# Optimization experiments

Hardware: AMD Instinct MI355X
Metric: run time of the kernel (lower is better)

The kernel has to match this reference:

```python
import jax, jax.numpy as jnp
import numpy as np

B, D, UNITS, T, M = 16384, 256, 256, 32, 64


def hard_sigmoid(x):
    # keras hard_sigmoid: clip(0.2*x + 0.5, 0, 1)
    return jnp.clip(0.2 * x + 0.5, 0.0, 1.0)


def setup_inputs() -> dict:
    key = jax.random.key(0)
    ks = jax.random.split(key, 11)
    inputs = jax.random.normal(ks[0], (B, D), jnp.float32)
    h_tm1 = jax.random.normal(ks[1], (B, UNITS), jnp.float32)
    c_tm1 = jax.random.normal(ks[2], (B, UNITS), jnp.float32)
    h_tm2 = jax.random.normal(ks[3], (B, UNITS), jnp.float32)
    c_tm2 = jax.random.normal(ks[4], (B, UNITS), jnp.float32)
    neighbors = jax.random.randint(ks[5], (B, T, M), 0, 2, jnp.int32)      # binary adjacency rows
    mapping = jax.random.randint(ks[6], (B, M), 0, T, jnp.int32)           # processing time of each node
    reverse_mapping = jax.random.randint(ks[7], (B, T), 0, T, jnp.int32)   # time -> row index in neighbors
    W = jax.random.normal(ks[8], (D, 4 * UNITS), jnp.float32) * 0.05
    U = jax.random.normal(ks[9], (UNITS, 4 * UNITS), jnp.float32) * 0.05
    Un = jax.random.normal(ks[10], (UNITS, 4 * UNITS), jnp.float32) * 0.05
    # unit_forget_bias: zeros for i, ones for f, zeros for c and o
    bias = jnp.concatenate([jnp.zeros((UNITS,)), jnp.ones((UNITS,)), jnp.zeros((2 * UNITS,))]).astype(jnp.float32)
    return {"inputs": inputs, "h_tm1": h_tm1, "c_tm1": c_tm1, "h_tm2": h_tm2, "c_tm2": c_tm2,
            "neighbors": neighbors, "mapping": mapping, "reverse_mapping": reverse_mapping,
            "time": 16, "W": W, "U": U, "Un": Un, "bias": bias}


def reference(inputs, h_tm1, c_tm1, h_tm2, c_tm2, neighbors, mapping, reverse_mapping, time, W, U, Un, bias):
    # --- neighbor row gather: ng_rows[b] = neighbors[b, reverse_mapping[b, time]] ---
    prev_pos = reverse_mapping[:, time]                                      # [B]
    ng_rows = jnp.take_along_axis(neighbors, prev_pos[:, None, None], axis=1)[:, 0, :]  # [B, M]
    ng_f = ng_rows.astype(jnp.float32)
    is_past = (mapping < time).astype(jnp.float32)                           # [B, M]
    ng_num = jnp.sum(ng_f, axis=-1)                                          # [B]
    cnt_past = jnp.sum(ng_f * is_past, axis=-1)                              # [B]
    cnt_fut = ng_num - cnt_past                                              # [B]
    denom = jnp.where(ng_num > 0, ng_num, 1.0)
    has_ng = (ng_num > 0)[:, None]

    # original sums the FULL-batch state for each neighbor (K.sum over axes [0,1]),
    # so aggregation collapses to count_past*sum(h_tm1) + count_fut*sum(h_tm2), div_no_nan by ng_num.
    hs1 = jnp.sum(h_tm1, axis=0)                                             # [units]
    hs2 = jnp.sum(h_tm2, axis=0)
    ngs = jnp.where(has_ng,
                    (cnt_past[:, None] * hs1[None, :] + cnt_fut[:, None] * hs2[None, :]) / denom[:, None],
                    0.0)                                                     # [B, units]

    # --- gates (implementation=1, no dropout) ---
    z_x = inputs @ W + bias                                                  # [B, 4*units]
    x_i, x_f, x_c, x_o = jnp.split(z_x, 4, axis=-1)                          # x_f_avg == x_f in source
    U_i, U_f, U_c, U_o = jnp.split(U, 4, axis=-1)
    Un_i, Un_f, Un_c, Un_o = jnp.split(Un, 4, axis=-1)

    i = hard_sigmoid(x_i + h_tm1 @ U_i + ngs @ Un_i)
    f_avg = hard_sigmoid(x_f + h_tm1 @ Un_f)   # note: uses Un_f per source
    f = hard_sigmoid(x_f + h_tm1 @ U_f)
    c = jnp.tanh(x_c + h_tm1 @ U_c + ngs @ Un_c)
    o = hard_sigmoid(x_o + h_tm1 @ U_o + ngs @ Un_o)

    # --- neighbor memory aggregation: same batch-summed structure with f_avg*c ---
    m1 = jnp.sum(f_avg * c_tm1, axis=0)                                      # [units]
    m2 = jnp.sum(f_avg * c_tm2, axis=0)
    mem_agg = jnp.where(has_ng,
                        (cnt_past[:, None] * m1[None, :] + cnt_fut[:, None] * m2[None, :]) / denom[:, None],
                        0.0)                                                 # [B, units]

    memory = mem_agg + f * c_tm1 + i * c
    h = o * jnp.tanh(memory)
    return h, memory
```

## Files before the change

### kernel.cpp

```cpp
#include <hip/hip_runtime.h>
#include <cmath>

#define BB 16384
#define DD 256
#define UU 256
#define TT 32
#define MM 64

#define WS_ALPHA 0
#define WS_BETA  16384
#define WS_M1    32768
#define WS_M2    33024
#define WS_V1    33280
#define WS_V2    34304
#define WS_PART1 35328
#define WS_PART2 68096
#define WS_BF16_BYTE 403456

typedef short bf16x8 __attribute__((ext_vector_type(8)));
typedef float f32x16 __attribute__((ext_vector_type(16)));

__device__ __forceinline__ float hsig(float x) {
    return fminf(1.0f, fmaxf(0.0f, fmaf(0.2f, x, 0.5f)));
}
__device__ __forceinline__ short f2bf(float x) {
    unsigned u = __float_as_uint(x);
    unsigned r = (u + 0x7fffu + ((u >> 16) & 1u)) >> 16;
    return (short)r;
}
__device__ __forceinline__ float bf2f(short h) {
    return __uint_as_float(((unsigned)(unsigned short)h) << 16);
}

__global__ void k_prep(const float* __restrict__ inputs, const float* __restrict__ h1,
                       const float* __restrict__ h2,
                       const int* __restrict__ neighbors, const int* __restrict__ mapping,
                       const int* __restrict__ revmap, const int* __restrict__ timep,
                       const float* __restrict__ W, const float* __restrict__ U,
                       const float* __restrict__ Un,
                       short* __restrict__ Ahi, short* __restrict__ Alo,
                       short* __restrict__ Bg,
                       float* __restrict__ alpha, float* __restrict__ beta,
                       float* __restrict__ part1, float* __restrict__ part2) {
    int blk = blockIdx.x;
    int tid = threadIdx.x;
    if (blk < 4096) {
        int q = tid & 3;
        int m = (blk & 255) * 64 + (tid >> 2);
        int kc = blk >> 8;
        int s = q >> 1, h = q & 1;
        int k0 = kc * 32 + s * 16 + h * 4;
        const float* src = (k0 < 256) ? (inputs + m * 256 + k0) : (h1 + m * 256 + k0 - 256);
        float4 x0 = *(const float4*)(src);
        float4 x1 = *(const float4*)(src + 8);
        float xs[8] = {x0.x, x0.y, x0.z, x0.w, x1.x, x1.y, x1.z, x1.w};
        bf16x8 hv, lv;
        #pragma unroll
        for (int j = 0; j < 8; j++) {
            short hh = f2bf(xs[j]);
            hv[j] = hh;
            lv[j] = f2bf(xs[j] - bf2f(hh));
        }
        long doff = ((long)kc * 16384 + m) * 32 + q * 8;
        *(bf16x8*)(Ahi + doff) = hv;
        *(bf16x8*)(Alo + doff) = lv;
    } else if (blk < 4416) {
        int t = (blk - 4096) * 256 + tid;
        int lane = t & 63;
        int rest = t >> 6;
        int gs = rest % 10;
        int img = rest / 10;
        int g = gs >> 1, s = gs & 1;
        int nb = img >> 4, kc = img & 15;
        int u = nb * 32 + (lane & 31);
        int hl = lane >> 5;
        int c = (g < 4) ? g * 256 + u : 256 + u;
        bf16x8 hv, lv;
        #pragma unroll
        for (int j = 0; j < 8; j++) {
            int k = kc * 32 + s * 16 + hl * 4 + (j & 3) + 8 * (j >> 2);
            const float* sp;
            if (k < 256) sp = W + k * 1024 + c;
            else         sp = ((g < 4) ? U : Un) + (k - 256) * 1024 + c;
            float x = *sp;
            short hh = f2bf(x);
            hv[j] = hh;
            lv[j] = f2bf(x - bf2f(hh));
        }
        short* dst = Bg + (long)img * 10240 + gs * 512 + lane * 8;
        *(bf16x8*)dst = hv;
        *(bf16x8*)(dst + 5120) = lv;
    } else if (blk < 8512) {
        int lane = tid & 63;
        int wid  = tid >> 6;
        int b = (blk - 4416) * 4 + wid;
        int t = timep[0];
        int p = revmap[b * TT + t];
        int ng = neighbors[(b * TT + p) * MM + lane];
        int mp = mapping[b * MM + lane];
        int cnt = ng;
        int cp  = (mp < t) ? ng : 0;
        #pragma unroll
        for (int off = 32; off > 0; off >>= 1) {
            cnt += __shfl_xor(cnt, off);
            cp  += __shfl_xor(cp, off);
        }
        if (lane == 0) {
            float a = 0.f, be = 0.f;
            if (cnt > 0) {
                float inv = 1.0f / (float)cnt;
                a  = (float)cp * inv;
                be = (float)(cnt - cp) * inv;
            }
            alpha[b] = a;
            beta[b]  = be;
        }
    } else {
        int p = blk - 8512;
        int r0 = p * 128;
        float s1 = 0.f, s2 = 0.f;
        for (int r = 0; r < 128; r++) {
            s1 += h1[(r0 + r) * UU + tid];
            s2 += h2[(r0 + r) * UU + tid];
        }
        part1[p * 256 + tid] = s1;
        part2[p * 256 + tid] = s2;
    }
}

__global__ void k_mid(const float* __restrict__ Un,
                      const float* __restrict__ part1, const float* __restrict__ part2,
                      float* __restrict__ v1, float* __restrict__ v2,
                      float* __restrict__ m12) {
    __shared__ float sh1[256], sh2[256];
    int tid = threadIdx.x;
    if (blockIdx.x == 0 && tid < 512) m12[tid] = 0.f;
    float s1 = 0.f, s2 = 0.f;
    #pragma unroll 8
    for (int p = 0; p < 128; p++) {
        s1 += part1[p * 256 + tid];
        s2 += part2[p * 256 + tid];
    }
    sh1[tid] = s1;
    sh2[tid] = s2;
    __syncthreads();
    int j = blockIdx.x * 256 + tid;
    float a1 = 0.f, a2 = 0.f;
    for (int k = 0; k < 256; k++) {
        float w = Un[k * 1024 + j];
        a1 = fmaf(sh1[k], w, a1);
        a2 = fmaf(sh2[k], w, a2);
    }
    v1[j] = a1;
    v2[j] = a2;
}

#define STAGE_B(KC, BUF) { \
    const char* _s = (const char*)(Bt + (long)(KC) * 10240); \
    char* _d = (char*)(&Bs[BUF][0]); \
    _Pragma("unroll") \
    for (int _c = 0; _c < 5; _c++) { \
        int _u = wv * 5120 + _c * 1024; \
        __builtin_amdgcn_global_load_lds( \
            (const __attribute__((address_space(1))) void*)(_s + _u + lane * 16), \
            (__attribute__((address_space(3))) void*)(_d + _u), 16, 0, 0); \
    } }

__global__ __launch_bounds__(256) void k_gemm_mfma(
    const short* __restrict__ Ahi, const short* __restrict__ Alo,
    const short* __restrict__ Bg,
    const float* __restrict__ c1p, const float* __restrict__ c2p,
    const float* __restrict__ bias,
    const float* __restrict__ alpha, const float* __restrict__ beta,
    const float* __restrict__ v1, const float* __restrict__ v2,
    float* __restrict__ m1, float* __restrict__ m2,
    float* __restrict__ out_h, float* __restrict__ out_mem)
{
    __shared__ short Bs[2][10240];

    const int tid = threadIdx.x;
    const int lane = tid & 63;
    const int wv = tid >> 6;
    const int mb = blockIdx.x;
    const int nb = blockIdx.y;
    const int m0 = mb * 128;
    const short* Bt = Bg + (long)nb * 163840;

    const int col = lane & 31;
    const int hl = lane >> 5;
    const int m = m0 + wv * 32 + col;
    const long abase = (long)m * 32 + hl * 8;

    f32x16 acc[5];
    #pragma unroll
    for (int g = 0; g < 5; g++)
        #pragma unroll
        for (int r = 0; r < 16; r++) acc[g][r] = 0.f;

    STAGE_B(0, 0);
    bf16x8 ah0 = *(const bf16x8*)(Ahi + abase);
    bf16x8 ah1 = *(const bf16x8*)(Ahi + abase + 16);
    bf16x8 al0 = *(const bf16x8*)(Alo + abase);
    bf16x8 al1 = *(const bf16x8*)(Alo + abase + 16);

    for (int kc = 0; kc < 16; kc++) {
        __syncthreads();
        bf16x8 nh0, nh1, nl0, nl1;
        if (kc + 1 < 16) {
            STAGE_B(kc + 1, (kc + 1) & 1);
            long ab = abase + (long)(kc + 1) * 524288;
            nh0 = *(const bf16x8*)(Ahi + ab);
            nh1 = *(const bf16x8*)(Ahi + ab + 16);
            nl0 = *(const bf16x8*)(Alo + ab);
            nl1 = *(const bf16x8*)(Alo + ab + 16);
        }

        const char* bp = (const char*)Bs + (kc & 1) * 20480 + lane * 16;
        #pragma unroll
        for (int g = 0; g < 5; g++) {
            bf16x8 bh0 = *(const bf16x8*)(bp + (g * 2 + 0) * 1024);
            bf16x8 bh1 = *(const bf16x8*)(bp + (g * 2 + 1) * 1024);
            bf16x8 bl0 = *(const bf16x8*)(bp + 10240 + (g * 2 + 0) * 1024);
            bf16x8 bl1 = *(const bf16x8*)(bp + 10240 + (g * 2 + 1) * 1024);
            acc[g] = __builtin_amdgcn_mfma_f32_32x32x16_bf16(ah0, bh0, acc[g], 0, 0, 0);
            acc[g] = __builtin_amdgcn_mfma_f32_32x32x16_bf16(ah1, bh1, acc[g], 0, 0, 0);
            acc[g] = __builtin_amdgcn_mfma_f32_32x32x16_bf16(al0, bh0, acc[g], 0, 0, 0);
            acc[g] = __builtin_amdgcn_mfma_f32_32x32x16_bf16(al1, bh1, acc[g], 0, 0, 0);
            acc[g] = __builtin_amdgcn_mfma_f32_32x32x16_bf16(ah0, bl0, acc[g], 0, 0, 0);
            acc[g] = __builtin_amdgcn_mfma_f32_32x32x16_bf16(ah1, bl1, acc[g], 0, 0, 0);
        }
        if (kc + 1 < 16) { ah0 = nh0; ah1 = nh1; al0 = nl0; al1 = nl1; }
    }

    int u = nb * 32 + col;
    float bi = bias[u], bfv = bias[256 + u], bc = bias[512 + u], bo = bias[768 + u];
    float v1i = v1[u], v1c = v1[512 + u], v1o = v1[768 + u];
    float v2i = v2[u], v2c = v2[512 + u], v2o = v2[768 + u];

    float pm1 = 0.f, pm2 = 0.f;
    #pragma unroll
    for (int r = 0; r < 16; r++) {
        int row = (r & 3) + 8 * (r >> 2) + 4 * hl;
        int b = m0 + wv * 32 + row;
        float al = alpha[b], be = beta[b];
        float c1 = c1p[b * 256 + u];
        float c2 = c2p[b * 256 + u];
        float zi  = acc[0][r] + bi + al * v1i + be * v2i;
        float zf  = acc[1][r] + bfv;
        float zc  = acc[2][r] + bc + al * v1c + be * v2c;
        float zo  = acc[3][r] + bo + al * v1o + be * v2o;
        float zfa = acc[4][r] + bfv;
        float ig = hsig(zi), fg = hsig(zf), og = hsig(zo), fav = hsig(zfa);
        float cg = tanhf(zc);
        out_mem[b * 256 + u] = fg * c1 + ig * cg;
        out_h[b * 256 + u]  = og;
        pm1 += fav * c1;
        pm2 += fav * c2;
    }

    pm1 += __shfl_xor(pm1, 32);
    pm2 += __shfl_xor(pm2, 32);
    __syncthreads();
    float* red = (float*)&Bs[0][0];
    if (hl == 0) {
        red[(wv * 2 + 0) * 32 + col] = pm1;
        red[(wv * 2 + 1) * 32 + col] = pm2;
    }
    __syncthreads();
    if (tid < 64) {
        int d = tid >> 5, ui = tid & 31;
        float s = 0.f;
        #pragma unroll
        for (int w = 0; w < 4; w++) s += red[(w * 2 + d) * 32 + ui];
        atomicAdd(((d == 0) ? m1 : m2) + nb * 32 + ui, s);
    }
}

__global__ void k_final(const float* __restrict__ alpha, const float* __restrict__ beta,
                        const float* __restrict__ m1, const float* __restrict__ m2,
                        float* __restrict__ out_h, float* __restrict__ out_mem) {
    int idx = blockIdx.x * 256 + threadIdx.x;
    int b  = idx >> 6;
    int uv = idx & 63;
    float4 mp = ((const float4*)out_mem)[idx];
    float4 ov = ((const float4*)out_h)[idx];
    float al = alpha[b], be = beta[b];
    float4 m1v = ((const float4*)m1)[uv];
    float4 m2v = ((const float4*)m2)[uv];
    float4 mem, h;
    mem.x = fmaf(al, m1v.x, fmaf(be, m2v.x, mp.x)); h.x = ov.x * tanhf(mem.x);
    mem.y = fmaf(al, m1v.y, fmaf(be, m2v.y, mp.y)); h.y = ov.y * tanhf(mem.y);
    mem.z = fmaf(al, m1v.z, fmaf(be, m2v.z, mp.z)); h.z = ov.z * tanhf(mem.z);
    mem.w = fmaf(al, m1v.w, fmaf(be, m2v.w, mp.w)); h.w = ov.w * tanhf(mem.w);
    ((float4*)out_mem)[idx] = mem;
    ((float4*)out_h)[idx]   = h;
}

extern "C" void kernel_launch(void* const* d_in, const int* in_sizes, int n_in,
                              void* d_out, int out_size, void* d_ws, size_t ws_size,
                              hipStream_t stream) {
    const float* inputs   = (const float*)d_in[0];
    const float* h_tm1    = (const float*)d_in[1];
    const float* c_tm1    = (const float*)d_in[2];
    const float* h_tm2    = (const float*)d_in[3];
    const float* c_tm2    = (const float*)d_in[4];
    const int*   neighbors= (const int*)d_in[5];
    const int*   mapping  = (const int*)d_in[6];
    const int*   revmap   = (const int*)d_in[7];
    const int*   timep    = (const int*)d_in[8];
    const float* W        = (const float*)d_in[9];
    const float* Uw       = (const float*)d_in[10];
    const float* Un       = (const float*)d_in[11];
    const float* bias     = (const float*)d_in[12];

    float* ws    = (float*)d_ws;
    float* alpha = ws + WS_ALPHA;
    float* beta  = ws + WS_BETA;
    float* m1    = ws + WS_M1;
    float* m2    = ws + WS_M2;
    float* v1    = ws + WS_V1;
    float* v2    = ws + WS_V2;
    float* part1 = ws + WS_PART1;
    float* part2 = ws + WS_PART2;

    short* Ahi = (short*)((char*)d_ws + WS_BF16_BYTE);
    short* Alo = Ahi + 8388608;
    short* Bg  = Alo + 8388608;

    float* out_h   = (float*)d_out;
    float* out_mem = out_h + BB * UU;

    k_prep<<<8640, 256, 0, stream>>>(inputs, h_tm1, h_tm2, neighbors, mapping, revmap,
                                     timep, W, Uw, Un, Ahi, Alo, Bg, alpha, beta,
                                     part1, part2);
    k_mid<<<4, 256, 0, stream>>>(Un, part1, part2, v1, v2, m1);

    dim3 g3(128, 8);
    k_gemm_mfma<<<g3, 256, 0, stream>>>(Ahi, Alo, Bg, c_tm1, c_tm2, bias,
                                        alpha, beta, v1, v2, m1, m2, out_h, out_mem);

    k_final<<<BB * UU / 4 / 256, 256, 0, stream>>>(alpha, beta, m1, m2, out_h, out_mem);
}
```

Before: 361.7 us.

## Interleave MFMA accumulators and replace syncthreads with explicit vmcnt waits

Reorders the inner k-loop so consecutive MFMAs target the five independent accumulators rather than issuing six dependent MFMAs into the same accumulator, which hides MFMA result latency. LDS B-fragment reads are split into batches that are loaded ahead of the MFMAs consuming them. The full __syncthreads is replaced by explicit s_waitcnt vmcnt counts plus s_barrier, with sched_barriers pinning the order of loads. This lets prefetched A global loads stay in flight across the barrier. The hand-chosen vmcnt values depend on exactly how many memory ops STAGE_B issues, and a miscount could cause stale-data races.

```diff
diff --git a/kernel.cpp b/kernel.cpp
--- a/kernel.cpp
+++ b/kernel.cpp
@@ -198,37 +198,93 @@
         for (int r = 0; r < 16; r++) acc[g][r] = 0.f;
 
     STAGE_B(0, 0);
+    __builtin_amdgcn_sched_barrier(0);
     bf16x8 ah0 = *(const bf16x8*)(Ahi + abase);
     bf16x8 ah1 = *(const bf16x8*)(Ahi + abase + 16);
     bf16x8 al0 = *(const bf16x8*)(Alo + abase);
     bf16x8 al1 = *(const bf16x8*)(Alo + abase + 16);
+    __builtin_amdgcn_sched_barrier(0);
 
     for (int kc = 0; kc < 16; kc++) {
-        __syncthreads();
+        asm volatile("s_waitcnt vmcnt(4)" ::: "memory");
+        __builtin_amdgcn_s_barrier();
+
         bf16x8 nh0, nh1, nl0, nl1;
         if (kc + 1 < 16) {
             STAGE_B(kc + 1, (kc + 1) & 1);
+            __builtin_amdgcn_sched_barrier(0);
             long ab = abase + (long)(kc + 1) * 524288;
             nh0 = *(const bf16x8*)(Ahi + ab);
             nh1 = *(const bf16x8*)(Ahi + ab + 16);
             nl0 = *(const bf16x8*)(Alo + ab);
             nl1 = *(const bf16x8*)(Alo + ab + 16);
+            __builtin_amdgcn_sched_barrier(0);
+            asm volatile("s_waitcnt vmcnt(9)" ::: "memory");
+        } else {
+            asm volatile("s_waitcnt vmcnt(0)" ::: "memory");
         }
 
         const char* bp = (const char*)Bs + (kc & 1) * 20480 + lane * 16;
-        #pragma unroll
-        for (int g = 0; g < 5; g++) {
-            bf16x8 bh0 = *(const bf16x8*)(bp + (g * 2 + 0) * 1024);
-            bf16x8 bh1 = *(const bf16x8*)(bp + (g * 2 + 1) * 1024);
-            bf16x8 bl0 = *(const bf16x8*)(bp + 10240 + (g * 2 + 0) * 1024);
-            bf16x8 bl1 = *(const bf16x8*)(bp + 10240 + (g * 2 + 1) * 1024);
-            acc[g] = __builtin_amdgcn_mfma_f32_32x32x16_bf16(ah0, bh0, acc[g], 0, 0, 0);
-            acc[g] = __builtin_amdgcn_mfma_f32_32x32x16_bf16(ah1, bh1, acc[g], 0, 0, 0);
-            acc[g] = __builtin_amdgcn_mfma_f32_32x32x16_bf16(al0, bh0, acc[g], 0, 0, 0);
-            acc[g] = __builtin_amdgcn_mfma_f32_32x32x16_bf16(al1, bh1, acc[g], 0, 0, 0);
-            acc[g] = __builtin_amdgcn_mfma_f32_32x32x16_bf16(ah0, bl0, acc[g], 0, 0, 0);
-            acc[g] = __builtin_amdgcn_mfma_f32_32x32x16_bf16(ah1, bl1, acc[g], 0, 0, 0);
-        }
+        bf16x8 p0, p1, p2, p3, p4, q0, q1, q2, q3, q4;
+        p0 = *(const bf16x8*)(bp + 0 * 1024);
+        p1 = *(const bf16x8*)(bp + 2 * 1024);
+        p2 = *(const bf16x8*)(bp + 4 * 1024);
+        p3 = *(const bf16x8*)(bp + 6 * 1024);
+        p4 = *(const bf16x8*)(bp + 8 * 1024);
+        q0 = *(const bf16x8*)(bp + 1 * 1024);
+        q1 = *(const bf16x8*)(bp + 3 * 1024);
+        q2 = *(const bf16x8*)(bp + 5 * 1024);
+        q3 = *(const bf16x8*)(bp + 7 * 1024);
+        q4 = *(const bf16x8*)(bp + 9 * 1024);
+
+        acc[0] = __builtin_amdgcn_mfma_f32_32x32x16_bf16(ah0, p0, acc[0], 0, 0, 0);
+        acc[1] = __builtin_amdgcn_mfma_f32_32x32x16_bf16(ah0, p1, acc[1], 0, 0, 0);
+        acc[2] = __builtin_amdgcn_mfma_f32_32x32x16_bf16(ah0, p2, acc[2], 0, 0, 0);
+        acc[3] = __builtin_amdgcn_mfma_f32_32x32x16_bf16(ah0, p3, acc[3], 0, 0, 0);
+        acc[4] = __builtin_amdgcn_mfma_f32_32x32x16_bf16(ah0, p4, acc[4], 0, 0, 0);
+
+        acc[0] = __builtin_amdgcn_mfma_f32_32x32x16_bf16(al0, p0, acc[0], 0, 0, 0);
+        acc[1] = __builtin_amdgcn_mfma_f32_32x32x16_bf16(al0, p1, acc[1], 0, 0, 0);
+        acc[2] = __builtin_amdgcn_mfma_f32_32x32x16_bf16(al0, p2, acc[2], 0, 0, 0);
+        acc[3] = __builtin_amdgcn_mfma_f32_32x32x16_bf16(al0, p3, acc[3], 0, 0, 0);
+        acc[4] = __builtin_amdgcn_mfma_f32_32x32x16_bf16(al0, p4, acc[4], 0, 0, 0);
+
+        p0 = *(const bf16x8*)(bp + 10240 + 0 * 1024);
+        p1 = *(const bf16x8*)(bp + 10240 + 2 * 1024);
+        p2 = *(const bf16x8*)(bp + 10240 + 4 * 1024);
+        p3 = *(const bf16x8*)(bp + 10240 + 6 * 1024);
+        p4 = *(const bf16x8*)(bp + 10240 + 8 * 1024);
+
+        acc[0] = __builtin_amdgcn_mfma_f32_32x32x16_bf16(ah1, q0, acc[0], 0, 0, 0);
+        acc[1] = __builtin_amdgcn_mfma_f32_32x32x16_bf16(ah1, q1, acc[1], 0, 0, 0);
+        acc[2] = __builtin_amdgcn_mfma_f32_32x32x16_bf16(ah1, q2, acc[2], 0, 0, 0);
+        acc[3] = __builtin_amdgcn_mfma_f32_32x32x16_bf16(ah1, q3, acc[3], 0, 0, 0);
+        acc[4] = __builtin_amdgcn_mfma_f32_32x32x16_bf16(ah1, q4, acc[4], 0, 0, 0);
+
+        acc[0] = __builtin_amdgcn_mfma_f32_32x32x16_bf16(al1, q0, acc[0], 0, 0, 0);
+        acc[1] = __builtin_amdgcn_mfma_f32_32x32x16_bf16(al1, q1, acc[1], 0, 0, 0);
+        acc[2] = __builtin_amdgcn_mfma_f32_32x32x16_bf16(al1, q2, acc[2], 0, 0, 0);
+        acc[3] = __builtin_amdgcn_mfma_f32_32x32x16_bf16(al1, q3, acc[3], 0, 0, 0);
+        acc[4] = __builtin_amdgcn_mfma_f32_32x32x16_bf16(al1, q4, acc[4], 0, 0, 0);
+
+        q0 = *(const bf16x8*)(bp + 10240 + 1 * 1024);
+        q1 = *(const bf16x8*)(bp + 10240 + 3 * 1024);
+        q2 = *(const bf16x8*)(bp + 10240 + 5 * 1024);
+        q3 = *(const bf16x8*)(bp + 10240 + 7 * 1024);
+        q4 = *(const bf16x8*)(bp + 10240 + 9 * 1024);
+
+        acc[0] = __builtin_amdgcn_mfma_f32_32x32x16_bf16(ah0, p0, acc[0], 0, 0, 0);
+        acc[1] = __builtin_amdgcn_mfma_f32_32x32x16_bf16(ah0, p1, acc[1], 0, 0, 0);
+        acc[2] = __builtin_amdgcn_mfma_f32_32x32x16_bf16(ah0, p2, acc[2], 0, 0, 0);
+        acc[3] = __builtin_amdgcn_mfma_f32_32x32x16_bf16(ah0, p3, acc[3], 0, 0, 0);
+        acc[4] = __builtin_amdgcn_mfma_f32_32x32x16_bf16(ah0, p4, acc[4], 0, 0, 0);
+
+        acc[0] = __builtin_amdgcn_mfma_f32_32x32x16_bf16(ah1, q0, acc[0], 0, 0, 0);
+        acc[1] = __builtin_amdgcn_mfma_f32_32x32x16_bf16(ah1, q1, acc[1], 0, 0, 0);
+        acc[2] = __builtin_amdgcn_mfma_f32_32x32x16_bf16(ah1, q2, acc[2], 0, 0, 0);
+        acc[3] = __builtin_amdgcn_mfma_f32_32x32x16_bf16(ah1, q3, acc[3], 0, 0, 0);
+        acc[4] = __builtin_amdgcn_mfma_f32_32x32x16_bf16(ah1, q4, acc[4], 0, 0, 0);
+
         if (kc + 1 < 16) { ah0 = nh0; ah1 = nh1; al0 = nl0; al1 = nl1; }
     }
 
```

Result: no change. 361.1 us (-0.2%).
